# Kernel tuning notes

Measured on AMD Instinct MI355X. Metric: run time of the kernel, lower is better.

## Reference

```python
import jax, jax.numpy as jnp
import numpy as np

N, IN_DIM, OUT_DIM = 8192, 256, 128
NEG_BIG = -9e15


def setup_inputs() -> dict:
    key = jax.random.key(0)
    k_x, k_a, k_w, k_att = jax.random.split(key, 4)
    X = jax.random.normal(k_x, (N, IN_DIM), dtype=jnp.float32)
    A = jax.random.randint(k_a, (N, N), 0, 2).astype(jnp.float32)
    # nn.Linear(in_dim, out_dim, bias=False): weight [out_dim, in_dim]
    W = jax.random.normal(k_w, (OUT_DIM, IN_DIM), dtype=jnp.float32) / np.sqrt(IN_DIM)
    # nn.Linear(out_dim, 1, bias=False): weight [1, out_dim] -> store as [out_dim]
    a_w = jax.random.normal(k_att, (OUT_DIM,), dtype=jnp.float32) / np.sqrt(OUT_DIM)
    return {"X": X, "A": A, "W": W, "a_w": a_w}


def reference(X, A, W, a_w):
    Wh = X @ W.T                                  # [N, out_dim]
    e = jax.nn.relu(Wh) @ a_w                      # [N]  (a(relu(Wh)).squeeze(-1))
    # NOTE: faithful to source: e broadcasts over rows -> score[i, j] = e[j]
    scores = jnp.where(A > 0, e[None, :], NEG_BIG)  # [N, N]
    attention = jax.nn.softmax(scores, axis=1)      # [N, N]
    h_prime = attention @ Wh                        # [N, out_dim]
    return jax.nn.relu(h_prime)
```

## Files before the change

kernel.cpp:

```cpp
#include <hip/hip_runtime.h>

typedef float        f32x4  __attribute__((ext_vector_type(4)));
typedef __bf16       bf16x8 __attribute__((ext_vector_type(8)));
typedef unsigned int u32x4  __attribute__((ext_vector_type(4)));

#define NN   8192
#define IND  256
#define OUTD 128
#define NB   144

__device__ __forceinline__ bf16x8 cvt2(f32x4 a, f32x4 b) {
  bf16x8 r;
  r[0]=(__bf16)a[0]; r[1]=(__bf16)a[1]; r[2]=(__bf16)a[2]; r[3]=(__bf16)a[3];
  r[4]=(__bf16)b[0]; r[5]=(__bf16)b[1]; r[6]=(__bf16)b[2]; r[7]=(__bf16)b[3];
  return r;
}

__global__ __launch_bounds__(128) void k1_wh_e(const float* __restrict__ X,
                                               const float* __restrict__ W,
                                               const float* __restrict__ aw,
                                               float* __restrict__ Wh,
                                               float* __restrict__ ev) {
  const int lane = threadIdx.x & 63;
  const int wave = threadIdx.x >> 6;
  const int nlo  = lane & 15;
  const int quad = lane >> 4;
  const int rowBase = blockIdx.x * 32 + wave * 16;

  const float* xp = X + (size_t)(rowBase + nlo) * IND + quad * 8;
  f32x4 acc[8];
#pragma unroll
  for (int nt = 0; nt < 8; ++nt) acc[nt] = f32x4{0.f, 0.f, 0.f, 0.f};

#pragma unroll
  for (int kb = 0; kb < IND; kb += 32) {
    f32x4 a0 = *(const f32x4*)(xp + kb);
    f32x4 a1 = *(const f32x4*)(xp + kb + 4);
    bf16x8 af = cvt2(a0, a1);
#pragma unroll
    for (int nt = 0; nt < 8; ++nt) {
      const float* wp = W + (size_t)(nt * 16 + nlo) * IND + kb + quad * 8;
      f32x4 b0 = *(const f32x4*)wp;
      f32x4 b1 = *(const f32x4*)(wp + 4);
      acc[nt] = __builtin_amdgcn_mfma_f32_16x16x32_bf16(af, cvt2(b0, b1), acc[nt], 0, 0, 0);
    }
  }
  float p0 = 0.f, p1 = 0.f, p2 = 0.f, p3 = 0.f;
#pragma unroll
  for (int nt = 0; nt < 8; ++nt) {
    const int col = nt * 16 + nlo;
    const float awc = aw[col];
    const int r0 = rowBase + quad * 4;
    float v0 = acc[nt][0], v1 = acc[nt][1], v2 = acc[nt][2], v3 = acc[nt][3];
    Wh[(size_t)(r0 + 0) * OUTD + col] = v0;
    Wh[(size_t)(r0 + 1) * OUTD + col] = v1;
    Wh[(size_t)(r0 + 2) * OUTD + col] = v2;
    Wh[(size_t)(r0 + 3) * OUTD + col] = v3;
    p0 += fmaxf(v0, 0.f) * awc;
    p1 += fmaxf(v1, 0.f) * awc;
    p2 += fmaxf(v2, 0.f) * awc;
    p3 += fmaxf(v3, 0.f) * awc;
  }
#pragma unroll
  for (int off = 8; off; off >>= 1) {
    p0 += __shfl_xor(p0, off, 64);
    p1 += __shfl_xor(p1, off, 64);
    p2 += __shfl_xor(p2, off, 64);
    p3 += __shfl_xor(p3, off, 64);
  }
  if (nlo == 0) {
    const int r0 = rowBase + quad * 4;
    ev[r0 + 0] = p0; ev[r0 + 1] = p1; ev[r0 + 2] = p2; ev[r0 + 3] = p3;
  }
}

__global__ __launch_bounds__(256) void k2_bt(const float* __restrict__ Wh,
                                             const float* __restrict__ ev,
                                             __bf16* __restrict__ Bt) {
  const int j = blockIdx.x * 256 + threadIdx.x;
  const float w = expf(ev[j]);
  const int n0 = blockIdx.y * 18;
#pragma unroll
  for (int i = 0; i < 18; ++i) {
    const int n = n0 + i;
    float v = 0.f;
    if (n < OUTD) v = w * Wh[(size_t)j * OUTD + n];
    else if (n == OUTD) v = w;
    Bt[(size_t)n * NN + j] = (__bf16)v;
  }
}

__global__ __launch_bounds__(256, 1) void k3_gemm(const float* __restrict__ Adj,
                                                  const __bf16* __restrict__ Bt,
                                                  float* __restrict__ out) {
  __shared__ float red[3][32][145];
  const int lane = threadIdx.x & 63;
  const int wave = threadIdx.x >> 6;
  const int nlo  = lane & 15;
  const int quad = lane >> 4;
  const int rowBase = blockIdx.x * 32;
  const int k0 = wave * 2048;

  f32x4 acc[2][9];
#pragma unroll
  for (int mm = 0; mm < 2; ++mm)
#pragma unroll
    for (int nt = 0; nt < 9; ++nt) acc[mm][nt] = f32x4{0.f, 0.f, 0.f, 0.f};

  const float*  ap0 = Adj + (size_t)(rowBase + nlo) * NN + quad * 8 + k0;
  const float*  ap1 = ap0 + (size_t)16 * NN;
  const __bf16* bp  = Bt + (size_t)nlo * NN + quad * 8 + k0;

  for (int kb = 0; kb < 2048; kb += 32) {
    f32x4 x0 = __builtin_nontemporal_load((const f32x4*)(ap0 + kb));
    f32x4 x1 = __builtin_nontemporal_load((const f32x4*)(ap0 + kb + 4));
    f32x4 y0 = __builtin_nontemporal_load((const f32x4*)(ap1 + kb));
    f32x4 y1 = __builtin_nontemporal_load((const f32x4*)(ap1 + kb + 4));
    u32x4 braw[9];
#pragma unroll
    for (int nt = 0; nt < 9; ++nt)
      braw[nt] = *(const u32x4*)(bp + (size_t)nt * 16 * NN + kb);
    bf16x8 af0 = cvt2(x0, x1);
    bf16x8 af1 = cvt2(y0, y1);
#pragma unroll
    for (int nt = 0; nt < 9; ++nt) {
      bf16x8 bfv = __builtin_bit_cast(bf16x8, braw[nt]);
      acc[0][nt] = __builtin_amdgcn_mfma_f32_16x16x32_bf16(af0, bfv, acc[0][nt], 0, 0, 0);
      acc[1][nt] = __builtin_amdgcn_mfma_f32_16x16x32_bf16(af1, bfv, acc[1][nt], 0, 0, 0);
    }
  }

  if (wave) {
    float (*slot)[145] = red[wave - 1];
#pragma unroll
    for (int mm = 0; mm < 2; ++mm)
#pragma unroll
      for (int nt = 0; nt < 9; ++nt)
#pragma unroll
        for (int rg = 0; rg < 4; ++rg)
          slot[mm * 16 + quad * 4 + rg][nt * 16 + nlo] = acc[mm][nt][rg];
  }
  __syncthreads();
  if (wave == 0) {
#pragma unroll
    for (int mm = 0; mm < 2; ++mm) {
#pragma unroll
      for (int nt = 0; nt < 9; ++nt)
#pragma unroll
        for (int rg = 0; rg < 4; ++rg) {
          const int r = mm * 16 + quad * 4 + rg;
          const int c = nt * 16 + nlo;
          acc[mm][nt][rg] += red[0][r][c] + red[1][r][c] + red[2][r][c];
        }
      float inv[4];
#pragma unroll
      for (int rg = 0; rg < 4; ++rg)
        inv[rg] = 1.0f / __shfl(acc[mm][8][rg], quad << 4, 64);
#pragma unroll
      for (int nt = 0; nt < 8; ++nt)
#pragma unroll
        for (int rg = 0; rg < 4; ++rg) {
          const int row = rowBase + mm * 16 + quad * 4 + rg;
          out[(size_t)row * OUTD + nt * 16 + nlo] = fmaxf(acc[mm][nt][rg] * inv[rg], 0.f);
        }
    }
  }
}

extern "C" void kernel_launch(void* const* d_in, const int* in_sizes, int n_in,
                              void* d_out, int out_size, void* d_ws, size_t ws_size,
                              hipStream_t stream) {
  const float* X  = (const float*)d_in[0];
  const float* A  = (const float*)d_in[1];
  const float* W  = (const float*)d_in[2];
  const float* aw = (const float*)d_in[3];
  float* out = (float*)d_out;

  char* ws = (char*)d_ws;
  float*  Wh = (float*)ws;
  float*  ev = (float*)(ws + 4194304);
  __bf16* Bt = (__bf16*)(ws + 4227072);

  k1_wh_e<<<256, 128, 0, stream>>>(X, W, aw, Wh, ev);
  k2_bt<<<dim3(32, 8), 256, 0, stream>>>(Wh, ev, Bt);
  k3_gemm<<<256, 256, 0, stream>>>(A, Bt, out);
}
```

Before: 462.5 us.

## Split main GEMM over K across blocks with separate reduction kernel

The adjacency-times-Bt GEMM now uses 16-row tiles and a 4-way split-K grid (2048 blocks instead of 256), with launch bounds allowing 4 blocks per CU. Partial sums, including the softmax denominator column, are written to a workspace buffer, and a new reduce kernel sums them, normalizes and applies ReLU. This raises occupancy and memory-level parallelism for streaming the 256MB fp32 adjacency matrix. The cost is extra partial-buffer traffic, an extra launch, and each Bt tile being reloaded by twice as many row blocks.

```diff
diff --git a/kernel.cpp b/kernel.cpp
--- a/kernel.cpp
+++ b/kernel.cpp
@@ -8,6 +8,7 @@
 #define IND  256
 #define OUTD 128
 #define NB   144
+#define KSPLIT 4
 
 __device__ __forceinline__ bf16x8 cvt2(f32x4 a, f32x4 b) {
   bf16x8 r;
@@ -90,81 +91,71 @@
   }
 }
 
-__global__ __launch_bounds__(256, 1) void k3_gemm(const float* __restrict__ Adj,
-                                                  const __bf16* __restrict__ Bt,
-                                                  float* __restrict__ out) {
-  __shared__ float red[3][32][145];
+__global__ __launch_bounds__(256, 4) void k3_partial(const float* __restrict__ Adj,
+                                                     const __bf16* __restrict__ Bt,
+                                                     float* __restrict__ part) {
+  __shared__ float red[3][16][145];
   const int lane = threadIdx.x & 63;
   const int wave = threadIdx.x >> 6;
   const int nlo  = lane & 15;
   const int quad = lane >> 4;
-  const int rowBase = blockIdx.x * 32;
-  const int k0 = wave * 2048;
+  const int rowBase = blockIdx.x * 16;
+  const int k0 = blockIdx.y * 2048 + wave * 512;
 
-  f32x4 acc[2][9];
+  f32x4 acc[9];
 #pragma unroll
-  for (int mm = 0; mm < 2; ++mm)
-#pragma unroll
-    for (int nt = 0; nt < 9; ++nt) acc[mm][nt] = f32x4{0.f, 0.f, 0.f, 0.f};
+  for (int nt = 0; nt < 9; ++nt) acc[nt] = f32x4{0.f, 0.f, 0.f, 0.f};
 
-  const float*  ap0 = Adj + (size_t)(rowBase + nlo) * NN + quad * 8 + k0;
-  const float*  ap1 = ap0 + (size_t)16 * NN;
-  const __bf16* bp  = Bt + (size_t)nlo * NN + quad * 8 + k0;
+  const float*  ap = Adj + (size_t)(rowBase + nlo) * NN + quad * 8 + k0;
+  const __bf16* bp = Bt + (size_t)nlo * NN + quad * 8 + k0;
 
-  for (int kb = 0; kb < 2048; kb += 32) {
-    f32x4 x0 = __builtin_nontemporal_load((const f32x4*)(ap0 + kb));
-    f32x4 x1 = __builtin_nontemporal_load((const f32x4*)(ap0 + kb + 4));
-    f32x4 y0 = __builtin_nontemporal_load((const f32x4*)(ap1 + kb));
-    f32x4 y1 = __builtin_nontemporal_load((const f32x4*)(ap1 + kb + 4));
+  for (int kb = 0; kb < 512; kb += 32) {
+    f32x4 x0 = __builtin_nontemporal_load((const f32x4*)(ap + kb));
+    f32x4 x1 = __builtin_nontemporal_load((const f32x4*)(ap + kb + 4));
     u32x4 braw[9];
 #pragma unroll
     for (int nt = 0; nt < 9; ++nt)
       braw[nt] = *(const u32x4*)(bp + (size_t)nt * 16 * NN + kb);
-    bf16x8 af0 = cvt2(x0, x1);
-    bf16x8 af1 = cvt2(y0, y1);
+    bf16x8 af = cvt2(x0, x1);
 #pragma unroll
-    for (int nt = 0; nt < 9; ++nt) {
-      bf16x8 bfv = __builtin_bit_cast(bf16x8, braw[nt]);
-      acc[0][nt] = __builtin_amdgcn_mfma_f32_16x16x32_bf16(af0, bfv, acc[0][nt], 0, 0, 0);
-      acc[1][nt] = __builtin_amdgcn_mfma_f32_16x16x32_bf16(af1, bfv, acc[1][nt], 0, 0, 0);
-    }
+    for (int nt = 0; nt < 9; ++nt)
+      acc[nt] = __builtin_amdgcn_mfma_f32_16x16x32_bf16(af, __builtin_bit_cast(bf16x8, braw[nt]), acc[nt], 0, 0, 0);
   }
 
   if (wave) {
     float (*slot)[145] = red[wave - 1];
 #pragma unroll
-    for (int mm = 0; mm < 2; ++mm)
+    for (int nt = 0; nt < 9; ++nt)
 #pragma unroll
-      for (int nt = 0; nt < 9; ++nt)
-#pragma unroll
-        for (int rg = 0; rg < 4; ++rg)
-          slot[mm * 16 + quad * 4 + rg][nt * 16 + nlo] = acc[mm][nt][rg];
+      for (int rg = 0; rg < 4; ++rg)
+        slot[quad * 4 + rg][nt * 16 + nlo] = acc[nt][rg];
   }
   __syncthreads();
   if (wave == 0) {
+    float* pbase = part + ((size_t)blockIdx.y * NN + rowBase) * NB;
 #pragma unroll
-    for (int mm = 0; mm < 2; ++mm) {
+    for (int nt = 0; nt < 9; ++nt)
 #pragma unroll
-      for (int nt = 0; nt < 9; ++nt)
+      for (int rg = 0; rg < 4; ++rg) {
+        const int r = quad * 4 + rg;
+        const int c = nt * 16 + nlo;
+        pbase[(size_t)r * NB + c] = acc[nt][rg] + red[0][r][c] + red[1][r][c] + red[2][r][c];
+      }
+  }
+}
+
+__global__ __launch_bounds__(256) void k3_reduce(const float* __restrict__ part,
+                                                 float* __restrict__ out) {
+  const int col = threadIdx.x & 127;
+  const int row = blockIdx.x * 2 + (threadIdx.x >> 7);
+  float num = 0.f, den = 0.f;
 #pragma unroll
-        for (int rg = 0; rg < 4; ++rg) {
-          const int r = mm * 16 + quad * 4 + rg;
-          const int c = nt * 16 + nlo;
-          acc[mm][nt][rg] += red[0][r][c] + red[1][r][c] + red[2][r][c];
-        }
-      float inv[4];
-#pragma unroll
-      for (int rg = 0; rg < 4; ++rg)
-        inv[rg] = 1.0f / __shfl(acc[mm][8][rg], quad << 4, 64);
-#pragma unroll
-      for (int nt = 0; nt < 8; ++nt)
-#pragma unroll
-        for (int rg = 0; rg < 4; ++rg) {
-          const int row = rowBase + mm * 16 + quad * 4 + rg;
-          out[(size_t)row * OUTD + nt * 16 + nlo] = fmaxf(acc[mm][nt][rg] * inv[rg], 0.f);
-        }
-    }
+  for (int s = 0; s < KSPLIT; ++s) {
+    const size_t base = ((size_t)s * NN + row) * NB;
+    num += part[base + col];
+    den += part[base + 128];
   }
+  out[(size_t)row * OUTD + col] = fmaxf(num / den, 0.f);
 }
 
 extern "C" void kernel_launch(void* const* d_in, const int* in_sizes, int n_in,
@@ -177,11 +168,13 @@
   float* out = (float*)d_out;
 
   char* ws = (char*)d_ws;
-  float*  Wh = (float*)ws;
-  float*  ev = (float*)(ws + 4194304);
-  __bf16* Bt = (__bf16*)(ws + 4227072);
+  float*  Wh   = (float*)ws;
+  float*  ev   = (float*)(ws + 4194304);
+  __bf16* Bt   = (__bf16*)(ws + 4227072);
+  float*  part = (float*)(ws + 8388608);
 
   k1_wh_e<<<256, 128, 0, stream>>>(X, W, aw, Wh, ev);
   k2_bt<<<dim3(32, 8), 256, 0, stream>>>(Wh, ev, Bt);
-  k3_gemm<<<256, 256, 0, stream>>>(A, Bt, out);
+  k3_partial<<<dim3(512, KSPLIT), 256, 0, stream>>>(A, Bt, part);
+  k3_reduce<<<4096, 256, 0, stream>>>(part, out);
 }
```

Result: slower. 518.6 us (+12.1%).
